# Performance work log

Hardware: AMD Instinct MI355X
Metric: run time of the kernel (lower is better)

## Reference

```python
import jax, jax.numpy as jnp
import numpy as np

# init kwargs (constants)
P = 1            # chamfer_distance_p
WEIGHT = 1.0
XYZ_UNIT = 0.1


def setup_inputs() -> dict:
    key = jax.random.key(0)
    k1, k2 = jax.random.split(key)
    B, N, M, D = 16, 4096, 4096, 3
    pred = jax.random.normal(k1, (B, N, D), dtype=jnp.float32)
    gt = jax.random.normal(k2, (B, M, D), dtype=jnp.float32)
    return {"pred": pred, "gt": gt}


def _chamfer(x, y, p):
    x2 = jnp.sum(x * x, axis=-1)                       # [B, N]
    y2 = jnp.sum(y * y, axis=-1)                       # [B, M]
    xy = jnp.einsum('bnd,bmd->bnm', x, y)              # [B, N, M]
    sq = jnp.maximum(x2[:, :, None] + y2[:, None, :] - 2.0 * xy, 0.0)
    dist = jnp.sqrt(sq)                                # torch.norm(x-y, dim=3)
    if p != 1:
        dist = dist ** p
    x_loss = jnp.mean(jnp.min(dist, axis=2), axis=1)   # [B]
    y_loss = jnp.mean(jnp.min(dist, axis=1), axis=1)   # [B]
    return jnp.mean(x_loss + y_loss)                   # scalar (reduce=True)


def reference(pred, gt):
    # HelperPointLoss.forward with reduce_over_batch=True, loss_name='chamfer_distance'
    loss = _chamfer(pred, gt, P)
    # info['helper_loss'] = loss (detached); info['helper_cderr'] = p=1 chamfer * xyz_unit
    cderr = _chamfer(pred, gt, 1) * XYZ_UNIT
    return (WEIGHT * loss, loss, cderr)
```

## Files before the change

kernel.cpp:

```cpp
#include <hip/hip_runtime.h>
#include <hip/hip_fp16.h>

typedef __attribute__((ext_vector_type(8)))  _Float16 half8;
typedef __attribute__((ext_vector_type(16))) float    f32x16;

#define B_   16
#define NPTS 4096

constexpr int BLK  = 512;
constexpr int WV   = 8;
constexpr int QF   = 2;
constexpr int TF   = 2;
constexpr int QPW  = 32 * QF;
constexpr int TSPL = 2;
constexpr int QG   = WV / TSPL;
constexpr int QPB  = QG * QPW;
constexpr int NQC  = NPTS / QPB;
constexpr int TPS  = NPTS / TSPL;
constexpr int TPW  = TPS / 32;
constexpr int NIT  = TPW / TF;
constexpr int NBLK = 2 * B_ * NQC;

__device__ __forceinline__ float min3f(float a, float b, float c) {
    return fminf(fminf(a, b), c);
}

__device__ __forceinline__ float tree16(const f32x16& d) {
    float a0 = min3f(d[0],  d[1],  d[2]);
    float a1 = min3f(d[3],  d[4],  d[5]);
    float a2 = min3f(d[6],  d[7],  d[8]);
    float a3 = min3f(d[9],  d[10], d[11]);
    float a4 = min3f(d[12], d[13], d[14]);
    return fminf(min3f(a0, a1, a2), min3f(a3, a4, d[15]));
}

__global__ __launch_bounds__(BLK, 4) void chamfer_mfma(
        const float* __restrict__ pred, const float* __restrict__ gt,
        float* __restrict__ accum, unsigned* __restrict__ counter,
        float* __restrict__ out) {
    const int qc  = blockIdx.x;
    const int b   = blockIdx.y;
    const int dir = blockIdx.z;
    const float* qsrc = dir ? gt   : pred;
    const float* tsrc = dir ? pred : gt;

    __shared__ uint4 sh[NPTS];
    __shared__ float sred[WV][QPW];
    __shared__ float ps[QG];

    const int tid  = threadIdx.x;
    const int lane = tid & 63;
    const int wv   = tid >> 6;
    const int m    = lane & 31;
    const int qg   = wv >> 1;
    const int ts   = wv & 1;

    const float* qbase = qsrc + (b * NPTS + qc * QPB + qg * QPW) * 3;
    half8 bfrag[QF];
    float q2[QF];
#pragma unroll
    for (int f = 0; f < QF; ++f) {
        const float* qp = qbase + (f * 32 + m) * 3;
        __half hqx = __float2half(qp[0]);
        __half hqy = __float2half(qp[1]);
        __half hqz = __float2half(qp[2]);
        float fqx = __half2float(hqx), fqy = __half2float(hqy), fqz = __half2float(hqz);
        q2[f] = fmaf(fqx, fqx, fmaf(fqy, fqy, fqz * fqz));
        uint4 bu;
        bu.x = (unsigned)__half_as_ushort(hqx) | ((unsigned)__half_as_ushort(hqy) << 16);
        bu.y = (unsigned)__half_as_ushort(hqz) | (0x3C00u << 16);
        bu.z = 0x3C00u;
        bu.w = 0u;
        bfrag[f] = __builtin_bit_cast(half8, bu);
    }

    f32x16 zero;
#pragma unroll
    for (int i = 0; i < 16; ++i) zero[i] = 0.0f;

    const float* tp = tsrc + b * NPTS * 3;
#pragma unroll
    for (int k = 0; k < NPTS / BLK; ++k) {
        int j = k * BLK + tid;
        __half hx = __float2half(tp[3 * j + 0]);
        __half hy = __float2half(tp[3 * j + 1]);
        __half hz = __float2half(tp[3 * j + 2]);
        float fx = __half2float(hx), fy = __half2float(hy), fz = __half2float(hz);
        float g2 = fmaf(fx, fx, fmaf(fy, fy, fz * fz));
        __half ax = __float2half(-2.0f * fx);
        __half ay = __float2half(-2.0f * fy);
        __half az = __float2half(-2.0f * fz);
        __half g2hi = __float2half(g2);
        __half g2lo = __float2half(g2 - __half2float(g2hi));
        uint4 w;
        w.x = (unsigned)__half_as_ushort(ax) | ((unsigned)__half_as_ushort(ay) << 16);
        w.y = (unsigned)__half_as_ushort(az) | ((unsigned)__half_as_ushort(g2hi) << 16);
        w.z = (unsigned)__half_as_ushort(g2lo);
        w.w = 0u;
        sh[j] = w;
    }
    __syncthreads();

    const uint4* shp = sh + ts * TPS + m;
    float mn0 = 1e30f, mn1 = 1e30f;
#pragma unroll 8
    for (int t = 0; t < NIT; ++t) {
        uint4 au0 = shp[t * 64];
        uint4 au1 = shp[t * 64 + 32];
        half8 a0 = __builtin_bit_cast(half8, au0);
        half8 a1 = __builtin_bit_cast(half8, au1);
        f32x16 d00 = __builtin_amdgcn_mfma_f32_32x32x16_f16(a0, bfrag[0], zero, 0, 0, 0);
        f32x16 d01 = __builtin_amdgcn_mfma_f32_32x32x16_f16(a0, bfrag[1], zero, 0, 0, 0);
        f32x16 d10 = __builtin_amdgcn_mfma_f32_32x32x16_f16(a1, bfrag[0], zero, 0, 0, 0);
        f32x16 d11 = __builtin_amdgcn_mfma_f32_32x32x16_f16(a1, bfrag[1], zero, 0, 0, 0);
        float t00 = tree16(d00);
        float t01 = tree16(d01);
        float t10 = tree16(d10);
        float t11 = tree16(d11);
        mn0 = min3f(mn0, t00, t10);
        mn1 = min3f(mn1, t01, t11);
    }

    float v0 = fminf(mn0, __shfl_xor(mn0, 32));
    float v1 = fminf(mn1, __shfl_xor(mn1, 32));
    float dd0 = fmaxf(fmaf(0.5f, v0, q2[0]), 0.0f);
    float dd1 = fmaxf(fmaf(0.5f, v1, q2[1]), 0.0f);
    if (lane < 32) {
        sred[wv][m]      = dd0;
        sred[wv][m + 32] = dd1;
    }
    __syncthreads();

    float s = 0.0f;
    if (wv < QG) {
        const int g  = wv;
        const int mm = lane;
        float d = fminf(sred[g * 2 + 0][mm], sred[g * 2 + 1][mm]);
        s = sqrtf(d);
#pragma unroll
        for (int off = 32; off; off >>= 1) s += __shfl_xor(s, off);
        if (lane == 0) ps[g] = s;
    }
    __syncthreads();

    if (tid == 0) {
        float bs = ps[0] + ps[1] + ps[2] + ps[3];
        atomicAdd(accum, bs);
        __threadfence();
        if (atomicAdd(counter, 1u) == NBLK - 1) {
            float total = atomicAdd(accum, 0.0f);
            float loss  = total * (1.0f / (float)(B_ * NPTS));
            out[0] = loss;
            out[1] = loss;
            out[2] = 0.1f * loss;
        }
    }
}

extern "C" void kernel_launch(void* const* d_in, const int* in_sizes, int n_in,
                              void* d_out, int out_size, void* d_ws, size_t ws_size,
                              hipStream_t stream) {
    const float* pred = (const float*)d_in[0];
    const float* gt   = (const float*)d_in[1];
    float*    out     = (float*)d_out;
    float*    accum   = (float*)d_ws;
    unsigned* counter = (unsigned*)d_ws + 1;

    hipMemsetAsync(d_ws, 0, 8, stream);
    chamfer_mfma<<<dim3(NQC, B_, 2), BLK, 0, stream>>>(pred, gt, accum, counter, out);
}
```

Before: 79.25 us.

## Precompute packed fp16 point fragments in a prep kernel and DMA them into LDS

Adds a prep kernel that converts every point once into packed fp16 MFMA A/B fragments and squared norms in workspace. The main kernel then fills shared memory with global_load_lds direct-to-LDS copies instead of each block redoing strided float loads and conversions for all 4096 target points. This removes redundant per-block conversion work and uncoalesced loads, at the cost of an extra kernel launch and a workspace round trip.

```diff
diff --git a/kernel.cpp b/kernel.cpp
--- a/kernel.cpp
+++ b/kernel.cpp
@@ -6,11 +6,11 @@
 
 #define B_   16
 #define NPTS 4096
+#define TPTS (B_ * NPTS)
 
 constexpr int BLK  = 512;
 constexpr int WV   = 8;
 constexpr int QF   = 2;
-constexpr int TF   = 2;
 constexpr int QPW  = 32 * QF;
 constexpr int TSPL = 2;
 constexpr int QG   = WV / TSPL;
@@ -18,7 +18,7 @@
 constexpr int NQC  = NPTS / QPB;
 constexpr int TPS  = NPTS / TSPL;
 constexpr int TPW  = TPS / 32;
-constexpr int NIT  = TPW / TF;
+constexpr int NIT  = TPW / 2;
 constexpr int NBLK = 2 * B_ * NQC;
 
 __device__ __forceinline__ float min3f(float a, float b, float c) {
@@ -34,15 +34,46 @@
     return fminf(min3f(a0, a1, a2), min3f(a3, a4, d[15]));
 }
 
+
+__global__ __launch_bounds__(512) void chamfer_prep(
+        const float* __restrict__ pred, const float* __restrict__ gt,
+        uint4* __restrict__ AF, uint2* __restrict__ BP, float* __restrict__ Q2) {
+    const int t = blockIdx.x >> 7;
+    const int i = (blockIdx.x & 127) * 512 + threadIdx.x;
+    const float* p = (t ? gt : pred) + i * 3;
+    __half hx = __float2half(p[0]);
+    __half hy = __float2half(p[1]);
+    __half hz = __float2half(p[2]);
+    float fx = __half2float(hx), fy = __half2float(hy), fz = __half2float(hz);
+    float g2 = fmaf(fx, fx, fmaf(fy, fy, fz * fz));
+    __half ax = __float2half(-2.0f * fx);
+    __half ay = __float2half(-2.0f * fy);
+    __half az = __float2half(-2.0f * fz);
+    __half g2hi = __float2half(g2);
+    __half g2lo = __float2half(g2 - __half2float(g2hi));
+    uint4 w;
+    w.x = (unsigned)__half_as_ushort(ax) | ((unsigned)__half_as_ushort(ay) << 16);
+    w.y = (unsigned)__half_as_ushort(az) | ((unsigned)__half_as_ushort(g2hi) << 16);
+    w.z = (unsigned)__half_as_ushort(g2lo);
+    w.w = 0u;
+    AF[t * TPTS + i] = w;
+    uint2 bp;
+    bp.x = (unsigned)__half_as_ushort(hx) | ((unsigned)__half_as_ushort(hy) << 16);
+    bp.y = (unsigned)__half_as_ushort(hz) | (0x3C00u << 16);
+    BP[t * TPTS + i] = bp;
+    Q2[t * TPTS + i] = g2;
+}
+
 __global__ __launch_bounds__(BLK, 4) void chamfer_mfma(
-        const float* __restrict__ pred, const float* __restrict__ gt,
+        const uint4* __restrict__ AF, const uint2* __restrict__ BP,
+        const float* __restrict__ Q2,
         float* __restrict__ accum, unsigned* __restrict__ counter,
         float* __restrict__ out) {
     const int qc  = blockIdx.x;
     const int b   = blockIdx.y;
     const int dir = blockIdx.z;
-    const float* qsrc = dir ? gt   : pred;
-    const float* tsrc = dir ? pred : gt;
+    const int qt  = dir;
+    const int tt  = dir ^ 1;
 
     __shared__ uint4 sh[NPTS];
     __shared__ float sred[WV][QPW];
@@ -55,20 +86,17 @@
     const int qg   = wv >> 1;
     const int ts   = wv & 1;
 
-    const float* qbase = qsrc + (b * NPTS + qc * QPB + qg * QPW) * 3;
+    const int qbase_i = qt * TPTS + b * NPTS + qc * QPB + qg * QPW;
     half8 bfrag[QF];
     float q2[QF];
 #pragma unroll
     for (int f = 0; f < QF; ++f) {
-        const float* qp = qbase + (f * 32 + m) * 3;
-        __half hqx = __float2half(qp[0]);
-        __half hqy = __float2half(qp[1]);
-        __half hqz = __float2half(qp[2]);
-        float fqx = __half2float(hqx), fqy = __half2float(hqy), fqz = __half2float(hqz);
-        q2[f] = fmaf(fqx, fqx, fmaf(fqy, fqy, fqz * fqz));
+        const int idx = qbase_i + f * 32 + m;
+        const uint2 bp = BP[idx];
+        q2[f] = Q2[idx];
         uint4 bu;
-        bu.x = (unsigned)__half_as_ushort(hqx) | ((unsigned)__half_as_ushort(hqy) << 16);
-        bu.y = (unsigned)__half_as_ushort(hqz) | (0x3C00u << 16);
+        bu.x = bp.x;
+        bu.y = bp.y;
         bu.z = 0x3C00u;
         bu.w = 0u;
         bfrag[f] = __builtin_bit_cast(half8, bu);
@@ -78,26 +106,13 @@
 #pragma unroll
     for (int i = 0; i < 16; ++i) zero[i] = 0.0f;
 
-    const float* tp = tsrc + b * NPTS * 3;
+    const uint4* afp = AF + tt * TPTS + b * NPTS;
 #pragma unroll
     for (int k = 0; k < NPTS / BLK; ++k) {
-        int j = k * BLK + tid;
-        __half hx = __float2half(tp[3 * j + 0]);
-        __half hy = __float2half(tp[3 * j + 1]);
-        __half hz = __float2half(tp[3 * j + 2]);
-        float fx = __half2float(hx), fy = __half2float(hy), fz = __half2float(hz);
-        float g2 = fmaf(fx, fx, fmaf(fy, fy, fz * fz));
-        __half ax = __float2half(-2.0f * fx);
-        __half ay = __float2half(-2.0f * fy);
-        __half az = __float2half(-2.0f * fz);
-        __half g2hi = __float2half(g2);
-        __half g2lo = __float2half(g2 - __half2float(g2hi));
-        uint4 w;
-        w.x = (unsigned)__half_as_ushort(ax) | ((unsigned)__half_as_ushort(ay) << 16);
-        w.y = (unsigned)__half_as_ushort(az) | ((unsigned)__half_as_ushort(g2hi) << 16);
-        w.z = (unsigned)__half_as_ushort(g2lo);
-        w.w = 0u;
-        sh[j] = w;
+        const int j = k * BLK + tid;
+        __builtin_amdgcn_global_load_lds(
+            (const __attribute__((address_space(1))) void*)(afp + j),
+            (__attribute__((address_space(3))) void*)(&sh[j]), 16, 0, 0);
     }
     __syncthreads();
 
@@ -165,7 +180,12 @@
     float*    out     = (float*)d_out;
     float*    accum   = (float*)d_ws;
     unsigned* counter = (unsigned*)d_ws + 1;
+    char*     base    = (char*)d_ws;
+    uint4*    AF      = (uint4*)(base + 1024);
+    uint2*    BP      = (uint2*)(base + 1024 + (2u << 20));
+    float*    Q2      = (float*)(base + 1024 + (3u << 20));
 
     hipMemsetAsync(d_ws, 0, 8, stream);
-    chamfer_mfma<<<dim3(NQC, B_, 2), BLK, 0, stream>>>(pred, gt, accum, counter, out);
+    chamfer_prep<<<dim3(256), dim3(512), 0, stream>>>(pred, gt, AF, BP, Q2);
+    chamfer_mfma<<<dim3(NQC, B_, 2), BLK, 0, stream>>>(AF, BP, Q2, accum, counter, out);
 }
```

After: 84.65 us. 1.07x slower.
